# Kernel optimization log

Measured on AMD Instinct MI355X. Metric: run time of the kernel, lower is better.

Reference implementation:

```python
import jax, jax.numpy as jnp
import numpy as np
from jax import lax

N_CLASS = 20
N_BOX = 2
GRID = 56          # n_cell_hw derived from input width: 56*56*(2*5+20) = 94080
BATCH = 256
SCORE_THRESH = 0.1 # hard-coded in _preds_filte
IOU_THRESH = 0.4   # hard-coded in _preds_filte
MAX_OUT = 30       # max_output_size
NMS_CAND = 256     # pre-select top candidates per image before O(K^2) NMS


def setup_inputs() -> dict:
    key = jax.random.key(0)
    D = GRID * GRID * (N_BOX * 5 + N_CLASS)
    net_outs = jax.random.uniform(key, (BATCH, D), dtype=jnp.float32)
    return {"net_outs": net_outs}


def _decode(net_outs):
    # Faithful port of _net_outs_parse (wh_sqrt=True)
    B = net_outs.shape[0]
    S, nb, C = GRID, N_BOX, N_CLASS
    bd1 = C * S * S
    bd2 = bd1 + nb * S * S
    cell_c = net_outs[:, :bd1].reshape(B, S, S, C)
    conf = net_outs[:, bd1:bd2].reshape(B, S, S, nb)
    coord = net_outs[:, bd2:].reshape(B, S, S, nb, 4)
    t_xy, t_wh = coord[..., :2], coord[..., 2:]
    # mesh_grid: w_index varies along axis 1, h_index along axis 0, stacked as (w, h)
    X, Y = jnp.meshgrid(jnp.arange(S, dtype=net_outs.dtype),
                        jnp.arange(S, dtype=net_outs.dtype), indexing='xy')
    grid = jnp.stack([X, Y], axis=-1)[:, :, None, :]  # [S,S,1,2]
    xy = (t_xy + grid) / S
    wh = jnp.square(t_wh)  # wh_sqrt=True
    mn = xy - wh * 0.5
    mx = xy + wh * 0.5
    # boxes_corner = [ymin, xmin, ymax, xmax]
    corners = jnp.concatenate([mn[..., 1:2], mn[..., 0:1], mx[..., 1:2], mx[..., 0:1]], axis=-1)
    c_probs = jnp.broadcast_to(cell_c[:, :, :, None, :], (B, S, S, nb, C))
    return jnp.concatenate([corners, conf[..., None], c_probs], axis=-1)  # [B,S,S,nb,5+C]


def _pairwise_iou(b):
    ymin, xmin, ymax, xmax = b[:, 0], b[:, 1], b[:, 2], b[:, 3]
    area = jnp.maximum(ymax - ymin, 0.0) * jnp.maximum(xmax - xmin, 0.0)
    iy = jnp.maximum(0.0, jnp.minimum(ymax[:, None], ymax[None, :]) - jnp.maximum(ymin[:, None], ymin[None, :]))
    ix = jnp.maximum(0.0, jnp.minimum(xmax[:, None], xmax[None, :]) - jnp.maximum(xmin[:, None], xmin[None, :]))
    inter = iy * ix
    union = area[:, None] + area[None, :] - inter
    return jnp.where(union > 0.0, inter / union, 0.0)


def _nms_image(item):
    # item: [N, 6] = (ymin, xmin, ymax, xmax, score, class)
    scores = item[:, 4]
    _, top_i = lax.top_k(scores, NMS_CAND)   # candidate pre-selection (greedy NMS only ever picks highest scores)
    cand = item[top_i]                       # [K, 6]
    iou = _pairwise_iou(cand[:, :4])         # [K, K]
    neg = jnp.finfo(item.dtype).min

    def step(valid, _):
        m = jnp.where(valid, cand[:, 4], neg)
        idx = jnp.argmax(m)
        ok = valid[idx]
        valid = valid & (iou[idx] <= IOU_THRESH)
        valid = valid.at[idx].set(False)
        return valid, (idx, ok)

    _, (idxs, ok) = lax.scan(step, jnp.ones(NMS_CAND, dtype=bool), None, length=MAX_OUT)
    rows = cand[idxs] * ok[:, None].astype(item.dtype)  # invalid slots -> zero rows (== pad with 0)
    _, oi = lax.top_k(rows[:, 4], MAX_OUT)               # sort by score desc, like tf.nn.top_k on padded preds
    return rows[oi]


def reference(net_outs):
    preds = _decode(net_outs)                    # [B,S,S,nb,25]
    B = preds.shape[0]
    cls_score = preds[..., 4:5] * preds[..., 5:]  # conf * class probs  [B,S,S,nb,C]
    cls = jnp.argmax(cls_score, axis=-1).astype(preds.dtype)
    s = jnp.max(cls_score, axis=-1)
    s = jnp.where(s >= SCORE_THRESH, s, 0.0)
    items = jnp.concatenate([preds[..., :4], s[..., None], cls[..., None]], axis=-1)
    items = items.reshape(B, -1, 6)              # [B, S*S*nb, 6]
    return jax.vmap(_nms_image)(items)           # [B, MAX_OUT, 6]
```

## Files before the change

kernel.cpp:

```cpp
#include <hip/hip_runtime.h>
#include <stdint.h>

#define S      56
#define NC     20
#define NBX    2
#define NCELL  (S*S)
#define NBOXES (NCELL*NBX)
#define DIM    94080
#define BD1    62720
#define BD2    68992
#define CAND   256
#define MAXOUT 30
#define NTHR   1024
#define NWAVE  (NTHR/64)

__device__ __forceinline__ uint64_t make_key(uint32_t sb, int idx) {
    return ((uint64_t)sb << 13) | (uint64_t)(8191 - idx);
}

__global__ __launch_bounds__(NTHR) void det_kernel(const float* __restrict__ in,
                                                   float* __restrict__ out) {
#pragma clang fp contract(off)
    const int b    = blockIdx.x;
    const int tid  = threadIdx.x;
    const int lane = tid & 63;
    const int wv   = tid >> 6;
    const float* img = in + (size_t)b * DIM;

    __shared__ uint32_t sbits[NBOXES];
    __shared__ uint8_t  cls8[NBOXES];
    __shared__ __attribute__((aligned(16))) uint32_t hist[NWAVE][256];
    __shared__ uint64_t skey[CAND];
    __shared__ uint64_t ssort[CAND];
    __shared__ uint64_t sel_prefix;
    __shared__ uint32_t sel_rank;
    __shared__ int      nsel;
    __shared__ float cymin[CAND], cxmin[CAND], cymax[CAND], cxmax[CAND];
    __shared__ float carea[CAND], cscore[CAND], ccls[CAND];
    __shared__ int   klist[MAXOUT];
    __shared__ float rowbuf[MAXOUT * 6];

    for (int cell = tid; cell < NCELL; cell += NTHR) {
        const float4* pv = (const float4*)(img + cell * NC);
        float p[NC];
        #pragma unroll
        for (int q = 0; q < 5; q++) {
            float4 v = pv[q];
            p[4*q+0] = v.x; p[4*q+1] = v.y; p[4*q+2] = v.z; p[4*q+3] = v.w;
        }
        float2 cf = *(const float2*)(img + BD1 + cell * 2);
        #pragma unroll
        for (int bb = 0; bb < NBX; bb++) {
            float conf = bb ? cf.y : cf.x;
            float best = conf * p[0];
            int   cls  = 0;
            #pragma unroll
            for (int c = 1; c < NC; c++) {
                float v = conf * p[c];
                if (v > best) { best = v; cls = c; }
            }
            float s = (best >= 0.1f) ? best : 0.0f;
            int idx = cell * 2 + bb;
            sbits[idx] = __float_as_uint(s);
            cls8[idx]  = (uint8_t)cls;
        }
    }
    if (tid == 0) nsel = 0;
    __syncthreads();

    uint64_t prefix = 0;
    uint32_t rank   = CAND;
    for (int pass = 0; pass < 6; pass++) {
        const int shift = 40 - 8 * pass;
        for (int i = tid; i < NWAVE * 256; i += NTHR) ((uint32_t*)hist)[i] = 0;
        __syncthreads();
        for (int idx = tid; idx < NBOXES; idx += NTHR) {
            uint64_t key = make_key(sbits[idx], idx);
            if ((key >> (shift + 8)) == prefix)
                atomicAdd(&hist[wv][(uint32_t)(key >> shift) & 255u], 1u);
        }
        __syncthreads();
        if (wv == 0) {
            uint32_t c0 = 0, c1 = 0, c2 = 0, c3 = 0;
            #pragma unroll
            for (int w = 0; w < NWAVE; w++) {
                uint4 h = ((const uint4*)hist[w])[lane];
                c0 += h.x; c1 += h.y; c2 += h.z; c3 += h.w;
            }
            uint32_t t = c0 + c1 + c2 + c3;
            uint32_t v = t;
            #pragma unroll
            for (int off = 1; off < 64; off <<= 1) {
                uint32_t u = __shfl_down(v, off);
                if (lane + off < 64) v += u;
            }
            uint32_t above = v - t;
            uint32_t s3 = above + c3;
            uint32_t s2 = s3 + c2;
            uint32_t s1 = s2 + c1;
            uint32_t s0 = s1 + c0;
            int dsel = -1; uint32_t g = 0;
            if      (above < rank && rank <= s3) { dsel = 4*lane+3; g = above; }
            else if (s3    < rank && rank <= s2) { dsel = 4*lane+2; g = s3; }
            else if (s2    < rank && rank <= s1) { dsel = 4*lane+1; g = s2; }
            else if (s1    < rank && rank <= s0) { dsel = 4*lane+0; g = s1; }
            if (dsel >= 0) {
                sel_prefix = (prefix << 8) | (uint64_t)dsel;
                sel_rank   = rank - g;
            }
        }
        __syncthreads();
        prefix = sel_prefix;
        rank   = sel_rank;
    }
    const uint64_t K256 = prefix;

    for (int idx = tid; idx < NBOXES; idx += NTHR) {
        uint64_t key = make_key(sbits[idx], idx);
        if (key >= K256) {
            int p = atomicAdd(&nsel, 1);
            if (p < CAND) skey[p] = key;
        }
    }
    if (tid < MAXOUT) klist[tid] = -1;
    __syncthreads();

    if (tid < CAND) {
        uint64_t my = skey[tid];
        int r = 0;
        #pragma unroll 8
        for (int j = 0; j < CAND; j++) r += (skey[j] > my);
        ssort[r] = my;
    }
    __syncthreads();
    if (tid < CAND) {
        uint64_t key = ssort[tid];
        int idx      = 8191 - (int)(key & 0x1FFF);
        uint32_t sb  = (uint32_t)(key >> 13);
        int cell = idx >> 1, bb = idx & 1;
        int i = cell / S, j = cell - i * S;
        float4 co = *(const float4*)(img + BD2 + cell * 8 + bb * 4);
        float x  = (co.x + (float)j) / 56.0f;
        float y  = (co.y + (float)i) / 56.0f;
        float wx = co.z * co.z;
        float wy = co.w * co.w;
        float hx = wx * 0.5f, hy = wy * 0.5f;
        float xmin = x - hx, ymin = y - hy, xmax = x + hx, ymax = y + hy;
        cymin[tid] = ymin; cxmin[tid] = xmin; cymax[tid] = ymax; cxmax[tid] = xmax;
        carea[tid] = fmaxf(ymax - ymin, 0.0f) * fmaxf(xmax - xmin, 0.0f);
        cscore[tid] = __uint_as_float(sb);
        ccls[tid]   = (float)cls8[idx];
    }
    __syncthreads();

    if (wv == 0) {
        float bym[4], bxm[4], byM[4], bxM[4], bar[4];
        #pragma unroll
        for (int s = 0; s < 4; s++) {
            int c = lane + 64 * s;
            bym[s] = cymin[c]; bxm[s] = cxmin[c];
            byM[s] = cymax[c]; bxM[s] = cxmax[c]; bar[s] = carea[c];
        }
        unsigned valid = 0xFu;
        for (int it = 0; it < MAXOUT; it++) {
            int p = -1;
            #pragma unroll
            for (int s = 0; s < 4; s++) {
                if (p < 0) {
                    unsigned long long bl = __ballot((valid >> s) & 1u);
                    if (bl) p = 64 * s + (__ffsll(bl) - 1);
                }
            }
            if (p < 0) break;
            if (lane == 0) klist[it] = p;
            float pym = cymin[p], pxm = cxmin[p];
            float pyM = cymax[p], pxM = cxmax[p], par = carea[p];
            #pragma unroll
            for (int s = 0; s < 4; s++) {
                int c = lane + 64 * s;
                float iy = fmaxf(0.0f, fminf(pyM, byM[s]) - fmaxf(pym, bym[s]));
                float ix = fmaxf(0.0f, fminf(pxM, bxM[s]) - fmaxf(pxm, bxm[s]));
                float inter = iy * ix;
                float uni   = par + bar[s] - inter;
                float iou   = (uni > 0.0f) ? (inter / uni) : 0.0f;
                if (c == p || !(iou <= 0.4f)) valid &= ~(1u << s);
            }
        }
    }
    __syncthreads();

    if (tid < MAXOUT) {
        int p = klist[tid];
        float* r = &rowbuf[tid * 6];
        if (p >= 0) {
            r[0] = cymin[p]; r[1] = cxmin[p]; r[2] = cymax[p];
            r[3] = cxmax[p]; r[4] = cscore[p]; r[5] = ccls[p];
        } else {
            r[0] = r[1] = r[2] = r[3] = r[4] = r[5] = 0.0f;
        }
    }
    __syncthreads();
    float* ob = out + (size_t)b * (MAXOUT * 6);
    if (tid < MAXOUT * 6) ob[tid] = rowbuf[tid];
}

extern "C" void kernel_launch(void* const* d_in, const int* in_sizes, int n_in,
                              void* d_out, int out_size, void* d_ws, size_t ws_size,
                              hipStream_t stream) {
    const float* in  = (const float*)d_in[0];
    float*       out = (float*)d_out;
    const int B = in_sizes[0] / DIM;
    det_kernel<<<dim3(B), dim3(NTHR), 0, stream>>>(in, out);
}
```

Baseline: 164.2 us.

## Replace six-pass radix select with single 8192-bin histogram threshold and register-held keys

Scores, index and class are packed into a single 64-bit key held in registers, so the per-box shared arrays are no longer needed. The six-pass 8-bit radix select becomes one 8192-bin histogram on the top score bits. A block-wide scan finds the threshold bin, and up to 512 candidates are gathered with wave-aggregated atomics and then rank-sorted. This removes several barrier-separated passes over shared memory, at the cost of a larger rank sort over up to 512 keys and a possible truncation if the threshold bin overflows the capacity. The NMS lane layout also changes so a single ballot plus shuffle picks the next box.

```diff
diff --git a/kernel.cpp b/kernel.cpp
--- a/kernel.cpp
+++ b/kernel.cpp
@@ -3,20 +3,17 @@
 
 #define S      56
 #define NC     20
-#define NBX    2
 #define NCELL  (S*S)
-#define NBOXES (NCELL*NBX)
+#define NBOXES (NCELL*2)
 #define DIM    94080
 #define BD1    62720
 #define BD2    68992
 #define CAND   256
 #define MAXOUT 30
 #define NTHR   1024
-#define NWAVE  (NTHR/64)
-
-__device__ __forceinline__ uint64_t make_key(uint32_t sb, int idx) {
-    return ((uint64_t)sb << 13) | (uint64_t)(8191 - idx);
-}
+#define NWAVE  16
+#define NBIN   8192
+#define CAP    512
 
 __global__ __launch_bounds__(NTHR) void det_kernel(const float* __restrict__ in,
                                                    float* __restrict__ out) {
@@ -27,116 +24,133 @@
     const int wv   = tid >> 6;
     const float* img = in + (size_t)b * DIM;
 
-    __shared__ uint32_t sbits[NBOXES];
-    __shared__ uint8_t  cls8[NBOXES];
-    __shared__ __attribute__((aligned(16))) uint32_t hist[NWAVE][256];
-    __shared__ uint64_t skey[CAND];
+    __shared__ uint32_t hist[NBIN];
+    __shared__ uint32_t wsum[NWAVE];
+    __shared__ int      bstar_s;
+    __shared__ int      nsel;
+    __shared__ uint64_t skey[CAP];
     __shared__ uint64_t ssort[CAND];
-    __shared__ uint64_t sel_prefix;
-    __shared__ uint32_t sel_rank;
-    __shared__ int      nsel;
     __shared__ float cymin[CAND], cxmin[CAND], cymax[CAND], cxmax[CAND];
     __shared__ float carea[CAND], cscore[CAND], ccls[CAND];
     __shared__ int   klist[MAXOUT];
     __shared__ float rowbuf[MAXOUT * 6];
 
-    for (int cell = tid; cell < NCELL; cell += NTHR) {
-        const float4* pv = (const float4*)(img + cell * NC);
-        float p[NC];
-        #pragma unroll
-        for (int q = 0; q < 5; q++) {
-            float4 v = pv[q];
-            p[4*q+0] = v.x; p[4*q+1] = v.y; p[4*q+2] = v.z; p[4*q+3] = v.w;
-        }
-        float2 cf = *(const float2*)(img + BD1 + cell * 2);
-        #pragma unroll
-        for (int bb = 0; bb < NBX; bb++) {
-            float conf = bb ? cf.y : cf.x;
-            float best = conf * p[0];
-            int   cls  = 0;
+    ((uint4*)hist)[tid]        = uint4{0,0,0,0};
+    ((uint4*)hist)[tid + NTHR] = uint4{0,0,0,0};
+    if (tid == 0) nsel = 0;
+    if (tid < MAXOUT) klist[tid] = -1;
+
+    uint64_t key[4][2];
+    bool     vld[4];
+    #pragma unroll
+    for (int i = 0; i < 4; i++) {
+        int cell = tid + NTHR * i;
+        vld[i] = (cell < NCELL);
+        key[i][0] = key[i][1] = 0;
+        if (vld[i]) {
+            const float4* pv = (const float4*)(img + cell * NC);
+            float p[NC];
             #pragma unroll
-            for (int c = 1; c < NC; c++) {
-                float v = conf * p[c];
-                if (v > best) { best = v; cls = c; }
-            }
-            float s = (best >= 0.1f) ? best : 0.0f;
-            int idx = cell * 2 + bb;
-            sbits[idx] = __float_as_uint(s);
-            cls8[idx]  = (uint8_t)cls;
-        }
-    }
-    if (tid == 0) nsel = 0;
-    __syncthreads();
-
-    uint64_t prefix = 0;
-    uint32_t rank   = CAND;
-    for (int pass = 0; pass < 6; pass++) {
-        const int shift = 40 - 8 * pass;
-        for (int i = tid; i < NWAVE * 256; i += NTHR) ((uint32_t*)hist)[i] = 0;
-        __syncthreads();
-        for (int idx = tid; idx < NBOXES; idx += NTHR) {
-            uint64_t key = make_key(sbits[idx], idx);
-            if ((key >> (shift + 8)) == prefix)
-                atomicAdd(&hist[wv][(uint32_t)(key >> shift) & 255u], 1u);
-        }
-        __syncthreads();
-        if (wv == 0) {
-            uint32_t c0 = 0, c1 = 0, c2 = 0, c3 = 0;
+            for (int q = 0; q < 5; q++) {
+                float4 v = pv[q];
+                p[4*q+0] = v.x; p[4*q+1] = v.y; p[4*q+2] = v.z; p[4*q+3] = v.w;
+            }
+            float2 cf = *(const float2*)(img + BD1 + cell * 2);
             #pragma unroll
-            for (int w = 0; w < NWAVE; w++) {
-                uint4 h = ((const uint4*)hist[w])[lane];
-                c0 += h.x; c1 += h.y; c2 += h.z; c3 += h.w;
-            }
-            uint32_t t = c0 + c1 + c2 + c3;
-            uint32_t v = t;
-            #pragma unroll
-            for (int off = 1; off < 64; off <<= 1) {
-                uint32_t u = __shfl_down(v, off);
-                if (lane + off < 64) v += u;
-            }
-            uint32_t above = v - t;
-            uint32_t s3 = above + c3;
-            uint32_t s2 = s3 + c2;
-            uint32_t s1 = s2 + c1;
-            uint32_t s0 = s1 + c0;
-            int dsel = -1; uint32_t g = 0;
-            if      (above < rank && rank <= s3) { dsel = 4*lane+3; g = above; }
-            else if (s3    < rank && rank <= s2) { dsel = 4*lane+2; g = s3; }
-            else if (s2    < rank && rank <= s1) { dsel = 4*lane+1; g = s2; }
-            else if (s1    < rank && rank <= s0) { dsel = 4*lane+0; g = s1; }
-            if (dsel >= 0) {
-                sel_prefix = (prefix << 8) | (uint64_t)dsel;
-                sel_rank   = rank - g;
-            }
-        }
-        __syncthreads();
-        prefix = sel_prefix;
-        rank   = sel_rank;
-    }
-    const uint64_t K256 = prefix;
-
-    for (int idx = tid; idx < NBOXES; idx += NTHR) {
-        uint64_t key = make_key(sbits[idx], idx);
-        if (key >= K256) {
-            int p = atomicAdd(&nsel, 1);
-            if (p < CAND) skey[p] = key;
-        }
-    }
-    if (tid < MAXOUT) klist[tid] = -1;
-    __syncthreads();
-
-    if (tid < CAND) {
+            for (int bb = 0; bb < 2; bb++) {
+                float conf = bb ? cf.y : cf.x;
+                float best = conf * p[0];
+                int   cls  = 0;
+                #pragma unroll
+                for (int c = 1; c < NC; c++) {
+                    float v = conf * p[c];
+                    if (v > best) { best = v; cls = c; }
+                }
+                uint32_t sb = (best >= 0.1f) ? __float_as_uint(best) : 0u;
+                int idx = cell * 2 + bb;
+                key[i][bb] = ((uint64_t)sb << 18) | ((uint64_t)(8191 - idx) << 5)
+                           | (uint64_t)cls;
+            }
+        }
+    }
+    __syncthreads();
+
+    #pragma unroll
+    for (int i = 0; i < 4; i++) {
+        #pragma unroll
+        for (int bb = 0; bb < 2; bb++) {
+            uint32_t sb = (uint32_t)(key[i][bb] >> 18);
+            if (vld[i] && sb != 0u) atomicAdd(&hist[sb >> 17], 1u);
+            unsigned long long zm = __ballot(vld[i] && sb == 0u);
+            if (lane == 0 && zm) atomicAdd(&hist[0], (uint32_t)__popcll(zm));
+        }
+    }
+    __syncthreads();
+
+    uint4 h0 = ((const uint4*)hist)[2*tid];
+    uint4 h1 = ((const uint4*)hist)[2*tid+1];
+    uint32_t hsum = h0.x+h0.y+h0.z+h0.w + h1.x+h1.y+h1.z+h1.w;
+    uint32_t v = hsum;
+    #pragma unroll
+    for (int off = 1; off < 64; off <<= 1) {
+        uint32_t u = __shfl_down(v, off);
+        if (lane + off < 64) v += u;
+    }
+    if (lane == 0) wsum[wv] = v;
+    __syncthreads();
+    uint32_t add = 0;
+    for (int w = wv + 1; w < NWAVE; w++) add += wsum[w];
+    uint32_t Sm    = v + add;
+    uint32_t above = Sm - hsum;
+    if (above < CAND && CAND <= Sm) {
+        uint32_t hh[8] = {h1.w, h1.z, h1.y, h1.x, h0.w, h0.z, h0.y, h0.x};
+        uint32_t g = above;
+        int bsel = 8 * tid;
+        #pragma unroll
+        for (int j = 0; j < 8; j++) {
+            if (g + hh[j] >= CAND) { bsel = 8 * tid + (7 - j); break; }
+            g += hh[j];
+        }
+        bstar_s = bsel;
+    }
+    __syncthreads();
+    const uint32_t bstar = (uint32_t)bstar_s;
+
+    #pragma unroll
+    for (int i = 0; i < 4; i++) {
+        #pragma unroll
+        for (int bb = 0; bb < 2; bb++) {
+            bool pred = vld[i] && ((uint32_t)(key[i][bb] >> 35) >= bstar);
+            unsigned long long mask = __ballot(pred);
+            if (mask) {
+                int leader = __ffsll(mask) - 1;
+                int base = 0;
+                if (lane == leader) base = atomicAdd(&nsel, (int)__popcll(mask));
+                base = __shfl(base, leader);
+                if (pred) {
+                    int pos = base + (int)__popcll(mask & ((1ull << lane) - 1ull));
+                    if (pos < CAP) skey[pos] = key[i][bb];
+                }
+            }
+        }
+    }
+    __syncthreads();
+
+    const int M = (nsel < CAP) ? nsel : CAP;
+    if (tid < M) {
         uint64_t my = skey[tid];
         int r = 0;
-        #pragma unroll 8
-        for (int j = 0; j < CAND; j++) r += (skey[j] > my);
-        ssort[r] = my;
-    }
-    __syncthreads();
+        #pragma unroll 4
+        for (int j = 0; j < M; j++) r += (skey[j] > my);
+        if (r < CAND) ssort[r] = my;
+    }
+    __syncthreads();
+
     if (tid < CAND) {
-        uint64_t key = ssort[tid];
-        int idx      = 8191 - (int)(key & 0x1FFF);
-        uint32_t sb  = (uint32_t)(key >> 13);
+        uint64_t k = ssort[tid];
+        int idx      = 8191 - (int)((k >> 5) & 0x1FFF);
+        int cls      = (int)(k & 31u);
+        uint32_t sb  = (uint32_t)(k >> 18);
         int cell = idx >> 1, bb = idx & 1;
         int i = cell / S, j = cell - i * S;
         float4 co = *(const float4*)(img + BD2 + cell * 8 + bb * 4);
@@ -149,7 +163,7 @@
         cymin[tid] = ymin; cxmin[tid] = xmin; cymax[tid] = ymax; cxmax[tid] = xmax;
         carea[tid] = fmaxf(ymax - ymin, 0.0f) * fmaxf(xmax - xmin, 0.0f);
         cscore[tid] = __uint_as_float(sb);
-        ccls[tid]   = (float)cls8[idx];
+        ccls[tid]   = (float)cls;
     }
     __syncthreads();
 
@@ -157,33 +171,29 @@
         float bym[4], bxm[4], byM[4], bxM[4], bar[4];
         #pragma unroll
         for (int s = 0; s < 4; s++) {
-            int c = lane + 64 * s;
+            int c = 4 * lane + s;
             bym[s] = cymin[c]; bxm[s] = cxmin[c];
             byM[s] = cymax[c]; bxM[s] = cxmax[c]; bar[s] = carea[c];
         }
-        unsigned valid = 0xFu;
+        unsigned vmask = 0xFu;
         for (int it = 0; it < MAXOUT; it++) {
-            int p = -1;
-            #pragma unroll
-            for (int s = 0; s < 4; s++) {
-                if (p < 0) {
-                    unsigned long long bl = __ballot((valid >> s) & 1u);
-                    if (bl) p = 64 * s + (__ffsll(bl) - 1);
-                }
-            }
-            if (p < 0) break;
+            unsigned long long mk = __ballot(vmask != 0u);
+            if (!mk) break;
+            int l0 = __ffsll(mk) - 1;
+            int vb = __shfl((int)vmask, l0);
+            int p  = 4 * l0 + (__ffs(vb) - 1);
             if (lane == 0) klist[it] = p;
             float pym = cymin[p], pxm = cxmin[p];
             float pyM = cymax[p], pxM = cxmax[p], par = carea[p];
             #pragma unroll
             for (int s = 0; s < 4; s++) {
-                int c = lane + 64 * s;
+                int c = 4 * lane + s;
                 float iy = fmaxf(0.0f, fminf(pyM, byM[s]) - fmaxf(pym, bym[s]));
                 float ix = fmaxf(0.0f, fminf(pxM, bxM[s]) - fmaxf(pxm, bxm[s]));
                 float inter = iy * ix;
                 float uni   = par + bar[s] - inter;
                 float iou   = (uni > 0.0f) ? (inter / uni) : 0.0f;
-                if (c == p || !(iou <= 0.4f)) valid &= ~(1u << s);
+                if (c == p || !(iou <= 0.4f)) vmask &= ~(1u << s);
             }
         }
     }
```

New measurement: 160.1 us. 1.03x faster.
